# Optimization experiments

Measured on AMD Instinct MI355X. Metric: run time of the kernel, lower is better.

## Reference

```python
import jax, jax.numpy as jnp
import numpy as np

B, S, DIM, H, DH, DEPTH, NCLS = 4, 2048, 128, 8, 128, 2, 10
M = 128          # number of FAVOR+ random features
CHUNK = 128      # chunk size for causal linear attention
INNER = H * DH   # performer-pytorch: dim_head=dim -> inner_dim = heads*dim
FF = 4 * DIM


def layernorm(x, g, b, eps=1e-5):
    mu = jnp.mean(x, axis=-1, keepdims=True)
    var = jnp.mean((x - mu) ** 2, axis=-1, keepdims=True)
    return (x - mu) * jax.lax.rsqrt(var + eps) * g + b


def softmax_kernel(data, proj, is_query, eps=1e-4):
    # FAVOR+ positive softmax-kernel features. data: [B,H,S,DH], proj: [M,DH]
    norm = DH ** -0.25
    ratio = M ** -0.5
    d = data * norm
    dd = jnp.einsum('bhsd,md->bhsm', d, proj)
    diag = 0.5 * jnp.sum(d * d, axis=-1, keepdims=True)
    if is_query:
        stab = jnp.max(dd, axis=-1, keepdims=True)
    else:
        stab = jnp.max(dd, axis=(-2, -1), keepdims=True)
    stab = jax.lax.stop_gradient(stab)
    return ratio * (jnp.exp(dd - diag - stab) + eps)


def causal_linear_attention(qp, kp, v):
    # qp,kp: [B,H,S,M], v: [B,H,S,DH]; chunked prefix-sum causal linear attention
    b, h, s, m = qp.shape
    d = v.shape[-1]
    nc = s // CHUNK
    def to_chunks(t):
        return t.reshape(b, h, nc, CHUNK, -1).transpose(2, 0, 1, 3, 4)
    qc, kc, vc = to_chunks(qp), to_chunks(kp), to_chunks(v)
    tri = jnp.tril(jnp.ones((CHUNK, CHUNK), qp.dtype))
    def step(carry, inp):
        kv_sum, k_sum = carry           # [b,h,m,d], [b,h,m]
        qi, ki, vi = inp                # [b,h,CHUNK,*]
        attn = jnp.einsum('bhim,bhjm->bhij', qi, ki) * tri
        num = jnp.einsum('bhij,bhjd->bhid', attn, vi) \
            + jnp.einsum('bhim,bhmd->bhid', qi, kv_sum)
        den = jnp.sum(attn, axis=-1) + jnp.einsum('bhim,bhm->bhi', qi, k_sum)
        out = num / (den[..., None] + 1e-6)
        kv_sum = kv_sum + jnp.einsum('bhjm,bhjd->bhmd', ki, vi)
        k_sum = k_sum + jnp.sum(ki, axis=2)
        return (kv_sum, k_sum), out
    init = (jnp.zeros((b, h, m, d), qp.dtype), jnp.zeros((b, h, m), qp.dtype))
    _, out = jax.lax.scan(step, init, (qc, kc, vc))
    return out.transpose(1, 2, 0, 3, 4).reshape(b, h, s, d)


def setup_inputs():
    key = jax.random.key(0)
    ks = jax.random.split(key, 12)
    rng = np.random.default_rng(0)
    # sinusoidal positional encoding [S, DIM]
    pe = np.zeros((S, DIM), np.float32)
    pos = np.arange(S)[:, None].astype(np.float32)
    div = np.exp(np.arange(0, DIM, 2).astype(np.float32) * (-np.log(10000.0) / DIM))
    pe[:, 0::2] = np.sin(pos * div)
    pe[:, 1::2] = np.cos(pos * div)
    # orthogonal random feature projections per layer [DEPTH, M, DH]
    proj = np.stack([
        (np.linalg.qr(rng.standard_normal((DH, DH)))[0][:M] * np.sqrt(DH))
        for _ in range(DEPTH)
    ]).astype(np.float32)
    def gn(k, shape, scale):
        return jax.random.normal(k, shape, jnp.float32) * scale
    return {
        'x': gn(ks[0], (B, S, 1), 1.0),
        'lin_w': gn(ks[1], (1, DIM), 1.0),
        'lin_b': jnp.zeros((DIM,), jnp.float32),
        'pe': jnp.asarray(pe),
        'proj': jnp.asarray(proj),
        'ln1_g': jnp.ones((DEPTH, DIM), jnp.float32),
        'ln1_b': jnp.zeros((DEPTH, DIM), jnp.float32),
        'wq': gn(ks[2], (DEPTH, DIM, INNER), DIM ** -0.5),
        'wk': gn(ks[3], (DEPTH, DIM, INNER), DIM ** -0.5),
        'wv': gn(ks[4], (DEPTH, DIM, INNER), DIM ** -0.5),
        'wo': gn(ks[5], (DEPTH, INNER, DIM), INNER ** -0.5),
        'wo_b': jnp.zeros((DEPTH, DIM), jnp.float32),
        'ln2_g': jnp.ones((DEPTH, DIM), jnp.float32),
        'ln2_b': jnp.zeros((DEPTH, DIM), jnp.float32),
        'ff1_w': gn(ks[6], (DEPTH, DIM, FF), DIM ** -0.5),
        'ff1_b': jnp.zeros((DEPTH, FF), jnp.float32),
        'ff2_w': gn(ks[7], (DEPTH, FF, DIM), FF ** -0.5),
        'ff2_b': jnp.zeros((DEPTH, DIM), jnp.float32),
        'fin_w': gn(ks[8], (DIM, NCLS), DIM ** -0.5),
        'fin_b': jnp.zeros((NCLS,), jnp.float32),
    }


def reference(x, lin_w, lin_b, pe, proj, ln1_g, ln1_b, wq, wk, wv, wo, wo_b,
              ln2_g, ln2_b, ff1_w, ff1_b, ff2_w, ff2_b, fin_w, fin_b):
    h = x @ lin_w + lin_b            # [B,S,DIM]
    h = h + pe[None]
    for l in range(DEPTH):
        # --- pre-norm FAVOR+ causal self-attention ---
        y = layernorm(h, ln1_g[l], ln1_b[l])
        def split(t):  # [B,S,INNER] -> [B,H,S,DH]
            return t.reshape(B, S, H, DH).transpose(0, 2, 1, 3)
        q, k, v = split(y @ wq[l]), split(y @ wk[l]), split(y @ wv[l])
        qp = softmax_kernel(q, proj[l], True)
        kp = softmax_kernel(k, proj[l], False)
        o = causal_linear_attention(qp, kp, v)          # [B,H,S,DH]
        o = o.transpose(0, 2, 1, 3).reshape(B, S, INNER)
        h = h + (o @ wo[l] + wo_b[l])
        # --- pre-norm FFN ---
        y = layernorm(h, ln2_g[l], ln2_b[l])
        f = jax.nn.gelu(y @ ff1_w[l] + ff1_b[l]) @ ff2_w[l] + ff2_b[l]
        h = h + f
    pooled = jnp.mean(h, axis=1)     # [B,DIM]
    return pooled @ fin_w + fin_b    # [B,NCLS]
```

## Files before the change

### kernel.cpp

```cpp
#include <hip/hip_runtime.h>
#include <hip/hip_bf16.h>

#define Bb 4
#define Ss 2048
#define DIMc 128
#define Hh 8
#define DHc 128
#define Mf 128
#define CH 128
#define NCc 16
#define INNERc 1024
#define FFc 512

union F4 { float4 v; float f[4]; };
typedef unsigned short u16;

typedef __bf16 bf16x8 __attribute__((ext_vector_type(8)));
typedef float  f32x4  __attribute__((ext_vector_type(4)));

__device__ __forceinline__ unsigned fkey(float f){
  unsigned b = __float_as_uint(f);
  return (b & 0x80000000u) ? ~b : (b | 0x80000000u);
}
__device__ __forceinline__ float funkey(unsigned u){
  unsigned b = (u & 0x80000000u) ? (u & 0x7fffffffu) : ~u;
  return __uint_as_float(b);
}
__device__ __forceinline__ float gelu_f(float x){
  return 0.5f*x*(1.0f + tanhf(0.7978845608028654f*(x + 0.044715f*x*x*x)));
}
__device__ __forceinline__ u16 f2bu(float f){
  unsigned u = __float_as_uint(f);
  return (u16)((u + 0x7fffu + ((u>>16)&1u)) >> 16);
}
__device__ __forceinline__ float b2f(u16 u){
  return __uint_as_float(((unsigned)u)<<16);
}

__device__ __forceinline__ bf16x8 ldfrag(const u16* base, int row, int e){
  int byte = (row*256 + e*2) ^ ((row&7)<<4);
  return *(const bf16x8*)((const char*)base + byte);
}
__device__ __forceinline__ void stage_lin_bf(u16* dst, const u16* src, int srs, int t){
  #pragma unroll
  for(int it=0; it<8; ++it){
    int idx = t + it*256; int r = idx>>4, c8 = idx&15;
    int byte = (r*256 + c8*16) ^ ((r&7)<<4);
    *(uint4*)((char*)dst + byte) = *(const uint4*)(src + r*srs + c8*8);
  }
}
__device__ __forceinline__ void stage_lin_f32(u16* dst, const float* src, int srs, int t){
  #pragma unroll
  for(int it=0; it<8; ++it){
    int idx = t + it*256; int r = idx>>4, c8 = idx&15;
    F4 v0, v1;
    v0.v = *(const float4*)(src + r*srs + c8*8);
    v1.v = *(const float4*)(src + r*srs + c8*8 + 4);
    u16 tmp[8];
    #pragma unroll
    for(int u=0;u<4;u++){ tmp[u] = f2bu(v0.f[u]); tmp[4+u] = f2bu(v1.f[u]); }
    int byte = (r*256 + c8*16) ^ ((r&7)<<4);
    *(uint4*)((char*)dst + byte) = *(uint4*)tmp;
  }
}
__device__ __forceinline__ void stage_tr_bf(u16* dst, const u16* src, int srs, int t){
  int j0 = (t & 63)*2; int wv = t>>6;
  #pragma unroll
  for(int it=0; it<2; ++it){
    int d0 = wv*16 + it*64;
    u16 a0[16], a1[16];
    *(uint4*)&a0[0] = *(const uint4*)(src + j0*srs + d0);
    *(uint4*)&a0[8] = *(const uint4*)(src + j0*srs + d0 + 8);
    *(uint4*)&a1[0] = *(const uint4*)(src + (j0+1)*srs + d0);
    *(uint4*)&a1[8] = *(const uint4*)(src + (j0+1)*srs + d0 + 8);
    #pragma unroll
    for(int dc=0; dc<16; ++dc){
      int d = d0 + dc;
      unsigned pk = (unsigned)a0[dc] | ((unsigned)a1[dc]<<16);
      int byte = (d*256 + j0*2) ^ ((d&7)<<4);
      *(unsigned*)((char*)dst + byte) = pk;
    }
  }
}
__device__ __forceinline__ void stage_tr_f32(u16* dst, const float* src, int srs, int t){
  int j0 = (t & 63)*2; int wv = t>>6;
  #pragma unroll
  for(int it=0; it<2; ++it){
    int d0 = wv*16 + it*64;
    F4 r0[4], r1[4];
    #pragma unroll
    for(int u=0;u<4;u++){
      r0[u].v = *(const float4*)(src + j0*srs     + d0 + u*4);
      r1[u].v = *(const float4*)(src + (j0+1)*srs + d0 + u*4);
    }
    #pragma unroll
    for(int dc=0; dc<16; ++dc){
      int d = d0 + dc;
      unsigned pk = (unsigned)f2bu(r0[dc>>2].f[dc&3]) |
                    ((unsigned)f2bu(r1[dc>>2].f[dc&3])<<16);
      int byte = (d*256 + j0*2) ^ ((d&7)<<4);
      *(unsigned*)((char*)dst + byte) = pk;
    }
  }
}

__device__ __forceinline__ int2 swz_tile(){
  int nx = gridDim.x;
  int nwg = gridDim.x*gridDim.y;
  int lin = blockIdx.y*nx + blockIdx.x;
  int q = nwg>>3, r = nwg&7;
  int xcd = lin&7, idx = lin>>3;
  int nl = (xcd<r) ? (xcd*(q+1)+idx) : (r*(q+1)+(xcd-r)*q+idx);
  return make_int2(nl % nx, nl / nx);
}

__global__ __launch_bounds__(64) void k_init(unsigned* kstab){
  if(threadIdx.x < 64) kstab[threadIdx.x] = 0u;
}

__global__ __launch_bounds__(256) void k_embed(const float* __restrict__ x,
    const float* __restrict__ lw, const float* __restrict__ lb,
    const float* __restrict__ pe, float* __restrict__ h){
  int idx = blockIdx.x*256 + threadIdx.x;
  int d = idx & 127; int bs = idx >> 7; int s = bs & (Ss-1);
  h[idx] = x[bs]*lw[d] + lb[d] + pe[s*DIMc + d];
}

__global__ __launch_bounds__(256) void k_ln(const float* __restrict__ in,
    const float* __restrict__ g, const float* __restrict__ bta,
    u16* __restrict__ out){
  int wave = threadIdx.x >> 6; int lane = threadIdx.x & 63;
  int row = blockIdx.x*4 + wave;
  const float* r = in + row*DIMc;
  float x1 = r[lane], x2 = r[lane+64];
  float s = x1+x2, sq = x1*x1 + x2*x2;
  #pragma unroll
  for(int m=1;m<64;m<<=1){ s += __shfl_xor(s,m,64); sq += __shfl_xor(sq,m,64); }
  float mu = s * (1.0f/128.0f);
  float var = sq*(1.0f/128.0f) - mu*mu;
  float rs = rsqrtf(var + 1e-5f);
  out[row*DIMc+lane]    = f2bu((x1-mu)*rs*g[lane]+bta[lane]);
  out[row*DIMc+lane+64] = f2bu((x2-mu)*rs*g[lane+64]+bta[lane+64]);
}

template<bool BIAS, bool GELU, bool RES, bool OBF>
__global__ __launch_bounds__(256) void k_gemm_bf(const u16* __restrict__ A,
    const float* __restrict__ Bw, const float* __restrict__ bias,
    const float* __restrict__ resid, void* __restrict__ Cp, int N, int K){
  __shared__ u16 As[64][40];
  __shared__ u16 Bs[64][40];
  int2 tt = swz_tile();
  int n0 = tt.x*64, m0 = tt.y*64;
  int t = threadIdx.x; int wid = t>>6, lane = t&63;
  int wr = wid>>1, wc = wid&1;
  int fr = lane&15, kc = lane>>4;
  f32x4 acc[2][2] = {};
  for(int k0=0; k0<K; k0+=32){
    {
      int r = t>>2, c8 = t&3;
      *(uint4*)&As[r][c8*8] = *(const uint4*)(A + (m0+r)*K + k0 + c8*8);
    }
    {
      int n = t&63, c8 = t>>6;
      u16 tmp[8];
      #pragma unroll
      for(int j=0;j<8;j++) tmp[j] = f2bu(Bw[(k0 + c8*8 + j)*N + n0 + n]);
      *(uint4*)&Bs[n][c8*8] = *(uint4*)tmp;
    }
    __syncthreads();
    bf16x8 af[2], bf[2];
    #pragma unroll
    for(int i=0;i<2;i++) af[i] = *(const bf16x8*)&As[wr*32 + i*16 + fr][kc*8];
    #pragma unroll
    for(int j=0;j<2;j++) bf[j] = *(const bf16x8*)&Bs[wc*32 + j*16 + fr][kc*8];
    #pragma unroll
    for(int i=0;i<2;i++)
      #pragma unroll
      for(int j=0;j<2;j++)
        acc[i][j] = __builtin_amdgcn_mfma_f32_16x16x32_bf16(af[i], bf[j], acc[i][j], 0, 0, 0);
    __syncthreads();
  }
  #pragma unroll
  for(int i=0;i<2;i++){
    #pragma unroll
    for(int r=0;r<4;r++){
      int row = m0 + wr*32 + i*16 + kc*4 + r;
      #pragma unroll
      for(int j=0;j<2;j++){
        int col = n0 + wc*32 + j*16 + fr;
        float val = acc[i][j][r];
        if(BIAS) val += bias[col];
        if(GELU) val = gelu_f(val);
        if(RES)  val += resid[row*N+col];
        if(OBF) ((u16*)Cp)[row*N+col] = f2bu(val);
        else    ((float*)Cp)[row*N+col] = val;
      }
    }
  }
}

template<bool ISQ>
__global__ __launch_bounds__(256) void k_featm(
    const u16* xin, u16* qout, float* ktmp,
    const float* __restrict__ proj, unsigned* kstab){
  __shared__ __align__(16) u16 xs[16384];
  __shared__ __align__(16) u16 ps[16384];
  __shared__ float diag_s[128];
  __shared__ unsigned hmax[8];
  int r0 = blockIdx.x*128;
  int t = threadIdx.x; int lane = t&63, w = t>>6;
  int fr = lane&15, kc = lane>>4;
  const float norm  = 0.29730177875068026f;
  const float ratio = 0.08838834764831845f;
  if(!ISQ && t<8) hmax[t] = 0u;
  stage_lin_bf(xs, xin + (size_t)r0*128, 128, t);
  stage_lin_f32(ps, proj, 128, t);
  {
    int r = t>>1, half = t&1;
    const u16* rp = xin + (size_t)(r0+r)*128 + half*64;
    float ss = 0.f;
    #pragma unroll
    for(int u4=0; u4<8; ++u4){
      u16 tmp[8]; *(uint4*)tmp = *(const uint4*)(rp + u4*8);
      #pragma unroll
      for(int u=0;u<8;u++){ float f = b2f(tmp[u]); ss += f*f; }
    }
    ss += __shfl_xor(ss, 1, 64);
    if(half==0) diag_s[r] = 0.5f*norm*norm*ss;
  }
  __syncthreads();
  f32x4 acc[2][8] = {};
  #pragma unroll
  for(int ks=0; ks<4; ++ks){
    bf16x8 a[2];
    #pragma unroll
    for(int i=0;i<2;i++) a[i] = ldfrag(xs, w*32+i*16+fr, ks*32+kc*8);
    bf16x8 bm[8];
    #pragma unroll
    for(int cb=0;cb<8;cb++) bm[cb] = ldfrag(ps, cb*16+fr, ks*32+kc*8);
    #pragma unroll
    for(int i=0;i<2;i++)
      #pragma unroll
      for(int cb=0;cb<8;cb++)
        acc[i][cb] = __builtin_amdgcn_mfma_f32_16x16x32_bf16(a[i], bm[cb], acc[i][cb], 0,0,0);
  }
  __syncthreads();
  #pragma unroll
  for(int i=0;i<2;i++){
    #pragma unroll
    for(int r=0;r<4;r++){
      int row = w*32 + i*16 + kc*4 + r;
      float rmax = acc[i][0][r];
      #pragma unroll
      for(int cb=1;cb<8;cb++) rmax = fmaxf(rmax, acc[i][cb][r]);
      #pragma unroll
      for(int msk=1;msk<16;msk<<=1) rmax = fmaxf(rmax, __shfl_xor(rmax, msk, 64));
      float dg = diag_s[row];
      if(ISQ){
        float base = -dg - norm*rmax;
        #pragma unroll
        for(int cb=0;cb<8;cb++){
          float val = ratio*(expf(fmaf(norm, acc[i][cb][r], base)) + 1e-4f);
          int byte = (row*256 + (cb*16+fr)*2) ^ ((row&7)<<4);
          *(u16*)((char*)xs + byte) = f2bu(val);
        }
      } else {
        if(fr==0) atomicMax(&hmax[row&7], fkey(norm*rmax));
        float* kb = ktmp + (size_t)(r0+row)*128;
        #pragma unroll
        for(int cb=0;cb<8;cb++)
          kb[cb*16+fr] = fmaf(norm, acc[i][cb][r], -dg);
      }
    }
  }
  __syncthreads();
  if(ISQ){
    #pragma unroll
    for(int it=0; it<8; ++it){
      int idx = t + it*256; int r = idx>>4, c8 = idx&15;
      int byte = (r*256 + c8*16) ^ ((r&7)<<4);
      *(uint4*)(qout + (size_t)(r0+r)*128 + c8*8) = *(uint4*)((char*)xs + byte);
    }
  } else {
    int b = r0 >> 14;
    if(t<8) atomicMax(&kstab[b*8 + t], hmax[t]);
  }
}

__global__ __launch_bounds__(256) void k_kfeatB(const float* __restrict__ ktmp,
    u16* __restrict__ kp, const unsigned* __restrict__ kstab){
  const float ratio = 0.08838834764831845f;
  int idx8 = blockIdx.x*256 + threadIdx.x;
  int e = idx8*8;
  int row = e >> 7; int bh = ((row>>14)<<3) | (row & 7);
  float stab = funkey(kstab[bh]);
  F4 v0, v1;
  v0.v = *(const float4*)(ktmp+e);
  v1.v = *(const float4*)(ktmp+e+4);
  u16 ob[8];
  #pragma unroll
  for(int u=0;u<4;u++) ob[u]   = f2bu(ratio*(expf(v0.f[u] - stab)+1e-4f));
  #pragma unroll
  for(int u=0;u<4;u++) ob[4+u] = f2bu(ratio*(expf(v1.f[u] - stab)+1e-4f));
  *(uint4*)(kp+e) = *(uint4*)ob;
}

__global__ __launch_bounds__(256) void k_attn1m(const u16* __restrict__ kp,
    const u16* __restrict__ v, float* __restrict__ kvc, float* __restrict__ ksc){
  __shared__ __align__(16) u16 kt[16384];
  __shared__ __align__(16) u16 vt[16384];
  int bc = blockIdx.x; int c = bc&15, bh = bc>>4, b = bh>>3, hh = bh&7;
  int t = threadIdx.x; int lane = t&63, w = t>>6;
  int fr = lane&15, kc = lane>>4;
  int s0 = c*128;
  const u16* kb = kp + (size_t)((b*Ss+s0)*Hh + hh)*128;
  const u16* vb = v  + (size_t)((b*Ss+s0)*Hh + hh)*128;
  stage_tr_bf(kt, kb, 1024, t);
  stage_tr_bf(vt, vb, 1024, t);
  __syncthreads();
  f32x4 acc[2][8] = {};
  f32x4 ks[2] = {};
  bf16x8 bones;
  #pragma unroll
  for(int e=0;e<8;e++) bones[e] = (fr==0) ? (__bf16)1.0f : (__bf16)0.0f;
  #pragma unroll
  for(int js=0;js<4;js++){
    bf16x8 am[2];
    #pragma unroll
    for(int i=0;i<2;i++) am[i] = ldfrag(kt, w*32+i*16+fr, js*32+kc*8);
    bf16x8 bv[8];
    #pragma unroll
    for(int cb=0;cb<8;cb++) bv[cb] = ldfrag(vt, cb*16+fr, js*32+kc*8);
    #pragma unroll
    for(int i=0;i<2;i++){
      ks[i] = __builtin_amdgcn_mfma_f32_16x16x32_bf16(am[i], bones, ks[i], 0,0,0);
      #pragma unroll
      for(int cb=0;cb<8;cb++)
        acc[i][cb] = __builtin_amdgcn_mfma_f32_16x16x32_bf16(am[i], bv[cb], acc[i][cb], 0,0,0);
    }
  }
  float* kvb = kvc + (size_t)bc*16384;
  #pragma unroll
  for(int i=0;i<2;i++){
    #pragma unroll
    for(int r=0;r<4;r++){
      int m = w*32 + i*16 + kc*4 + r;
      #pragma unroll
      for(int cb=0;cb<8;cb++) kvb[m*128 + cb*16 + fr] = acc[i][cb][r];
      if(fr==0) ksc[bc*128 + m] = ks[i][r];
    }
  }
}

__global__ __launch_bounds__(256) void k_prefix(float* __restrict__ kvc){
  int bh = blockIdx.x >> 6; int pos = (blockIdx.x & 63)*256 + threadIdx.x;
  int base = bh*16*16384 + pos;
  float a = 0.f;
  #pragma unroll
  for(int c=0;c<16;c++){
    float xv = kvc[base + c*16384];
    kvc[base + c*16384] = a;
    a += xv;
  }
}
__global__ __launch_bounds__(256) void k_prefix_ks(float* __restrict__ ksc){
  int e = blockIdx.x*256 + threadIdx.x;
  int bh = e>>7, m = e&127;
  float a = 0.f;
  #pragma unroll
  for(int c=0;c<16;c++){
    int idx = (bh*16+c)*128 + m;
    float xv = ksc[idx]; ksc[idx] = a; a += xv;
  }
}

__global__ __launch_bounds__(256) void k_attn2m(const u16* __restrict__ qp,
    const u16* __restrict__ kp, const u16* __restrict__ v,
    const float* __restrict__ kvc, const float* __restrict__ ksc,
    u16* __restrict__ o){
  __shared__ __align__(16) u16 qs[16384];
  __shared__ __align__(16) u16 bs[16384];
  __shared__ float ksum_s[128];
  int bc = blockIdx.x; int c = bc&15, bh = bc>>4, b = bh>>3, hh = bh&7;
  int t = threadIdx.x; int lane = t&63, w = t>>6;
  int fr = lane&15, kc = lane>>4;
  int s0 = c*128;
  const u16* qb = qp + (size_t)((b*Ss+s0)*Hh + hh)*128;
  const u16* kb = kp + (size_t)((b*Ss+s0)*Hh + hh)*128;
  const u16* vb = v  + (size_t)((b*Ss+s0)*Hh + hh)*128;
  const float* kvb = kvc + (size_t)bc*16384;
  stage_lin_bf(qs, qb, 1024, t);
  stage_lin_bf(bs, kb, 1024, t);
  if(t<128) ksum_s[t] = ksc[bc*128 + t];
  __syncthreads();
  bf16x8 aq[2][4];
  #pragma unroll
  for(int i=0;i<2;i++)
    #pragma unroll
    for(int ks=0;ks<4;ks++)
      aq[i][ks] = ldfrag(qs, w*32+i*16+fr, ks*32+kc*8);
  f32x4 sacc[2][8] = {};
  #pragma unroll
  for(int ks=0;ks<4;ks++){
    bf16x8 bk[8];
    #pragma unroll
    for(int cb=0;cb<8;cb++) bk[cb] = ldfrag(bs, cb*16+fr, ks*32+kc*8);
    #pragma unroll
    for(int i=0;i<2;i++)
      #pragma unroll
      for(int cb=0;cb<8;cb++)
        sacc[i][cb] = __builtin_amdgcn_mfma_f32_16x16x32_bf16(aq[i][ks], bk[cb], sacc[i][cb], 0,0,0);
  }
  __syncthreads();
  #pragma unroll
  for(int i=0;i<2;i++){
    #pragma unroll
    for(int cb=0;cb<8;cb++){
      #pragma unroll
      for(int r=0;r<4;r++){
        int prow = w*32 + i*16 + kc*4 + r;
        int pcol = cb*16 + fr;
        float pv = (pcol > prow) ? 0.f : sacc[i][cb][r];
        int byte = (prow*256 + pcol*2) ^ ((prow&7)<<4);
        *(u16*)((char*)qs + byte) = f2bu(pv);
      }
    }
  }
  stage_tr_bf(bs, vb, 1024, t);
  __syncthreads();
  f32x4 nacc[2][8] = {};
  f32x4 dacc[2] = {};
  bf16x8 bones;
  #pragma unroll
  for(int e=0;e<8;e++) bones[e] = (fr==0) ? (__bf16)1.0f : (__bf16)0.0f;
  #pragma unroll
  for(int js=0;js<4;js++){
    bf16x8 ap[2];
    #pragma unroll
    for(int i=0;i<2;i++) ap[i] = ldfrag(qs, w*32+i*16+fr, js*32+kc*8);
    bf16x8 bv[8];
    #pragma unroll
    for(int cb=0;cb<8;cb++) bv[cb] = ldfrag(bs, cb*16+fr, js*32+kc*8);
    #pragma unroll
    for(int i=0;i<2;i++){
      dacc[i] = __builtin_amdgcn_mfma_f32_16x16x32_bf16(ap[i], bones, dacc[i], 0,0,0);
      #pragma unroll
      for(int cb=0;cb<8;cb++)
        nacc[i][cb] = __builtin_amdgcn_mfma_f32_16x16x32_bf16(ap[i], bv[cb], nacc[i][cb], 0,0,0);
    }
  }
  __syncthreads();
  stage_tr_f32(bs, kvb, 128, t);
  __syncthreads();
  #pragma unroll
  for(int ms=0;ms<4;ms++){
    bf16x8 bkv[8];
    #pragma unroll
    for(int cb=0;cb<8;cb++) bkv[cb] = ldfrag(bs, cb*16+fr, ms*32+kc*8);
    bf16x8 bks;
    #pragma unroll
    for(int e=0;e<8;e++) bks[e] = (fr==0) ? (__bf16)ksum_s[ms*32+kc*8+e] : (__bf16)0.0f;
    #pragma unroll
    for(int i=0;i<2;i++){
      dacc[i] = __builtin_amdgcn_mfma_f32_16x16x32_bf16(aq[i][ms], bks, dacc[i], 0,0,0);
      #pragma unroll
      for(int cb=0;cb<8;cb++)
        nacc[i][cb] = __builtin_amdgcn_mfma_f32_16x16x32_bf16(aq[i][ms], bkv[cb], nacc[i][cb], 0,0,0);
    }
  }
  #pragma unroll
  for(int i=0;i<2;i++){
    #pragma unroll
    for(int r=0;r<4;r++){
      float den = __shfl(dacc[i][r], lane & 48, 64);
      float inv = 1.0f/(den + 1e-6f);
      int row = w*32 + i*16 + kc*4 + r;
      u16* ob = o + (size_t)((b*Ss+s0+row)*Hh + hh)*128;
      #pragma unroll
      for(int cb=0;cb<8;cb++)
        ob[cb*16 + fr] = f2bu(nacc[i][cb][r] * inv);
    }
  }
}

__global__ __launch_bounds__(256) void k_pool(const float* __restrict__ h,
    float* __restrict__ pw){
  __shared__ float part[256];
  int blk = blockIdx.x; int b = blk>>4, c = blk&15;
  int t = threadIdx.x; int half = t>>7;
  float s = 0.f;
  int s0 = c*128 + half*64;
  for(int si=s0; si<s0+64; ++si) s += h[(b*Ss+si)*128 + (t&127)];
  part[t] = s;
  __syncthreads();
  if(t<128) pw[blk*128 + t] = part[t] + part[t+128];
}
__global__ __launch_bounds__(128) void k_cls(const float* __restrict__ pw,
    const float* __restrict__ fw, const float* __restrict__ fb,
    float* __restrict__ out){
  __shared__ float pool_s[128];
  int b = blockIdx.x; int t = threadIdx.x;
  float s = 0.f;
  for(int c=0;c<16;c++) s += pw[(b*16+c)*128 + t];
  pool_s[t] = s * (1.0f/2048.0f);
  __syncthreads();
  if(t<10){
    float a = fb[t];
    for(int d=0; d<128; ++d) a += pool_s[d]*fw[d*10+t];
    out[b*10+t] = a;
  }
}

extern "C" void kernel_launch(void* const* d_in, const int* in_sizes, int n_in,
                              void* d_out, int out_size, void* d_ws, size_t ws_size,
                              hipStream_t stream){
  (void)in_sizes; (void)n_in; (void)out_size; (void)ws_size;
  const float* x     = (const float*)d_in[0];
  const float* lin_w = (const float*)d_in[1];
  const float* lin_b = (const float*)d_in[2];
  const float* pe    = (const float*)d_in[3];
  const float* proj  = (const float*)d_in[4];
  const float* ln1_g = (const float*)d_in[5];
  const float* ln1_b = (const float*)d_in[6];
  const float* wq    = (const float*)d_in[7];
  const float* wk    = (const float*)d_in[8];
  const float* wv    = (const float*)d_in[9];
  const float* wo    = (const float*)d_in[10];
  const float* wo_b  = (const float*)d_in[11];
  const float* ln2_g = (const float*)d_in[12];
  const float* ln2_b = (const float*)d_in[13];
  const float* ff1w  = (const float*)d_in[14];
  const float* ff1b  = (const float*)d_in[15];
  const float* ff2w  = (const float*)d_in[16];
  const float* ff2b  = (const float*)d_in[17];
  const float* finw  = (const float*)d_in[18];
  const float* finb  = (const float*)d_in[19];
  float* out = (float*)d_out;

  float* ws  = (float*)d_ws;
  float* h    = ws;
  u16*  y    = (u16*)(h + 1048576);
  u16*  q    = (u16*)(h + 1048576 + 524288);
  u16*  k    = q + 8388608;
  u16*  v    = k + 8388608;
  u16*  o    = v + 8388608;
  float* ktmp = (float*)(o + 8388608);
  float* kvc  = ktmp + 8388608;
  float* ksc  = kvc + 8388608;
  float* pw   = ksc + 65536;
  unsigned* kstab = (unsigned*)(pw + 8192);

  k_init<<<1,64,0,stream>>>(kstab);
  k_embed<<<4096,256,0,stream>>>(x, lin_w, lin_b, pe, h);
  for(int l=0;l<2;l++){
    const float* projl = proj + l*Mf*DHc;
    k_ln<<<2048,256,0,stream>>>(h, ln1_g + l*DIMc, ln1_b + l*DIMc, y);
    k_gemm_bf<false,false,false,true><<<dim3(16,128),256,0,stream>>>(y, wq + l*DIMc*INNERc, nullptr, nullptr, q, INNERc, DIMc);
    k_gemm_bf<false,false,false,true><<<dim3(16,128),256,0,stream>>>(y, wk + l*DIMc*INNERc, nullptr, nullptr, k, INNERc, DIMc);
    k_gemm_bf<false,false,false,true><<<dim3(16,128),256,0,stream>>>(y, wv + l*DIMc*INNERc, nullptr, nullptr, v, INNERc, DIMc);
    k_featm<true><<<512,256,0,stream>>>(q, q, nullptr, projl, nullptr);
    k_featm<false><<<512,256,0,stream>>>(k, nullptr, ktmp, projl, kstab + l*32);
    k_kfeatB<<<4096,256,0,stream>>>(ktmp, k, kstab + l*32);
    k_attn1m<<<512,256,0,stream>>>(k, v, kvc, ksc);
    k_prefix<<<2048,256,0,stream>>>(kvc);
    k_prefix_ks<<<16,256,0,stream>>>(ksc);
    k_attn2m<<<512,256,0,stream>>>(q, k, v, kvc, ksc, o);
    k_gemm_bf<true,false,true,false><<<dim3(2,128),256,0,stream>>>(o, wo + l*INNERc*DIMc, wo_b + l*DIMc, h, h, DIMc, INNERc);
    k_ln<<<2048,256,0,stream>>>(h, ln2_g + l*DIMc, ln2_b + l*DIMc, y);
    k_gemm_bf<true,true,false,true><<<dim3(8,128),256,0,stream>>>(y, ff1w + l*DIMc*FFc, ff1b + l*FFc, nullptr, q, FFc, DIMc);
    k_gemm_bf<true,false,true,false><<<dim3(2,128),256,0,stream>>>(q, ff2w + l*FFc*DIMc, ff2b + l*DIMc, h, h, DIMc, FFc);
  }
  k_pool<<<64,256,0,stream>>>(h, pw);
  k_cls<<<4,128,0,stream>>>(pw, finw, finb, out);
}
```

Baseline: 487.7 us.

## Defer key-feature stabilization into attention kernels and store KV chunk state in bf16

The key feature kernel now writes exp(dd - diag) directly as bf16 instead of an fp32 temporary. The global max stabilizer and the ratio/eps terms are applied later as a scale and offset when keys are staged in the attention kernels, which removes the separate k_kfeatB pass and its fp32 round trip. The per-chunk KV sums and their prefix scan are also moved from fp32 to bf16, halving that traffic and the number of prefix blocks. The costs are a possible fp32 exp overflow without pre-subtracting the max, and lower precision in the accumulated prefix state.

```diff
diff --git a/kernel.cpp b/kernel.cpp
--- a/kernel.cpp
+++ b/kernel.cpp
@@ -49,6 +49,18 @@
     *(uint4*)((char*)dst + byte) = *(const uint4*)(src + r*srs + c8*8);
   }
 }
+__device__ __forceinline__ void stage_lin_bf_s(u16* dst, const u16* src, int srs,
+    int t, float sc, float off){
+  #pragma unroll
+  for(int it=0; it<8; ++it){
+    int idx = t + it*256; int r = idx>>4, c8 = idx&15;
+    u16 tmp[8]; *(uint4*)tmp = *(const uint4*)(src + r*srs + c8*8);
+    #pragma unroll
+    for(int u=0;u<8;u++) tmp[u] = f2bu(fmaf(b2f(tmp[u]), sc, off));
+    int byte = (r*256 + c8*16) ^ ((r&7)<<4);
+    *(uint4*)((char*)dst + byte) = *(uint4*)tmp;
+  }
+}
 __device__ __forceinline__ void stage_lin_f32(u16* dst, const float* src, int srs, int t){
   #pragma unroll
   for(int it=0; it<8; ++it){
@@ -82,22 +94,22 @@
     }
   }
 }
-__device__ __forceinline__ void stage_tr_f32(u16* dst, const float* src, int srs, int t){
+__device__ __forceinline__ void stage_tr_bf_s(u16* dst, const u16* src, int srs,
+    int t, float sc, float off){
   int j0 = (t & 63)*2; int wv = t>>6;
   #pragma unroll
   for(int it=0; it<2; ++it){
     int d0 = wv*16 + it*64;
-    F4 r0[4], r1[4];
-    #pragma unroll
-    for(int u=0;u<4;u++){
-      r0[u].v = *(const float4*)(src + j0*srs     + d0 + u*4);
-      r1[u].v = *(const float4*)(src + (j0+1)*srs + d0 + u*4);
-    }
+    u16 a0[16], a1[16];
+    *(uint4*)&a0[0] = *(const uint4*)(src + j0*srs + d0);
+    *(uint4*)&a0[8] = *(const uint4*)(src + j0*srs + d0 + 8);
+    *(uint4*)&a1[0] = *(const uint4*)(src + (j0+1)*srs + d0);
+    *(uint4*)&a1[8] = *(const uint4*)(src + (j0+1)*srs + d0 + 8);
     #pragma unroll
     for(int dc=0; dc<16; ++dc){
       int d = d0 + dc;
-      unsigned pk = (unsigned)f2bu(r0[dc>>2].f[dc&3]) |
-                    ((unsigned)f2bu(r1[dc>>2].f[dc&3])<<16);
+      unsigned pk = (unsigned)f2bu(fmaf(b2f(a0[dc]), sc, off)) |
+                    ((unsigned)f2bu(fmaf(b2f(a1[dc]), sc, off))<<16);
       int byte = (d*256 + j0*2) ^ ((d&7)<<4);
       *(unsigned*)((char*)dst + byte) = pk;
     }
@@ -201,8 +213,7 @@
 
 template<bool ISQ>
 __global__ __launch_bounds__(256) void k_featm(
-    const u16* xin, u16* qout, float* ktmp,
-    const float* __restrict__ proj, unsigned* kstab){
+    const u16* xin, u16* qout, const float* __restrict__ proj, unsigned* kstab){
   __shared__ __align__(16) u16 xs[16384];
   __shared__ __align__(16) u16 ps[16384];
   __shared__ float diag_s[128];
@@ -250,12 +261,12 @@
     #pragma unroll
     for(int r=0;r<4;r++){
       int row = w*32 + i*16 + kc*4 + r;
+      float dg = diag_s[row];
       float rmax = acc[i][0][r];
       #pragma unroll
       for(int cb=1;cb<8;cb++) rmax = fmaxf(rmax, acc[i][cb][r]);
       #pragma unroll
       for(int msk=1;msk<16;msk<<=1) rmax = fmaxf(rmax, __shfl_xor(rmax, msk, 64));
-      float dg = diag_s[row];
       if(ISQ){
         float base = -dg - norm*rmax;
         #pragma unroll
@@ -266,56 +277,44 @@
         }
       } else {
         if(fr==0) atomicMax(&hmax[row&7], fkey(norm*rmax));
-        float* kb = ktmp + (size_t)(r0+row)*128;
         #pragma unroll
-        for(int cb=0;cb<8;cb++)
-          kb[cb*16+fr] = fmaf(norm, acc[i][cb][r], -dg);
+        for(int cb=0;cb<8;cb++){
+          float val = expf(fmaf(norm, acc[i][cb][r], -dg));
+          int byte = (row*256 + (cb*16+fr)*2) ^ ((row&7)<<4);
+          *(u16*)((char*)xs + byte) = f2bu(val);
+        }
       }
     }
   }
   __syncthreads();
-  if(ISQ){
-    #pragma unroll
-    for(int it=0; it<8; ++it){
-      int idx = t + it*256; int r = idx>>4, c8 = idx&15;
-      int byte = (r*256 + c8*16) ^ ((r&7)<<4);
-      *(uint4*)(qout + (size_t)(r0+r)*128 + c8*8) = *(uint4*)((char*)xs + byte);
-    }
-  } else {
+  #pragma unroll
+  for(int it=0; it<8; ++it){
+    int idx = t + it*256; int r = idx>>4, c8 = idx&15;
+    int byte = (r*256 + c8*16) ^ ((r&7)<<4);
+    *(uint4*)(qout + (size_t)(r0+r)*128 + c8*8) = *(uint4*)((char*)xs + byte);
+  }
+  if(!ISQ){
     int b = r0 >> 14;
     if(t<8) atomicMax(&kstab[b*8 + t], hmax[t]);
   }
 }
 
-__global__ __launch_bounds__(256) void k_kfeatB(const float* __restrict__ ktmp,
-    u16* __restrict__ kp, const unsigned* __restrict__ kstab){
-  const float ratio = 0.08838834764831845f;
-  int idx8 = blockIdx.x*256 + threadIdx.x;
-  int e = idx8*8;
-  int row = e >> 7; int bh = ((row>>14)<<3) | (row & 7);
-  float stab = funkey(kstab[bh]);
-  F4 v0, v1;
-  v0.v = *(const float4*)(ktmp+e);
-  v1.v = *(const float4*)(ktmp+e+4);
-  u16 ob[8];
-  #pragma unroll
-  for(int u=0;u<4;u++) ob[u]   = f2bu(ratio*(expf(v0.f[u] - stab)+1e-4f));
-  #pragma unroll
-  for(int u=0;u<4;u++) ob[4+u] = f2bu(ratio*(expf(v1.f[u] - stab)+1e-4f));
-  *(uint4*)(kp+e) = *(uint4*)ob;
-}
-
 __global__ __launch_bounds__(256) void k_attn1m(const u16* __restrict__ kp,
-    const u16* __restrict__ v, float* __restrict__ kvc, float* __restrict__ ksc){
+    const u16* __restrict__ v, u16* __restrict__ kvc, float* __restrict__ ksc,
+    const unsigned* __restrict__ kstab){
   __shared__ __align__(16) u16 kt[16384];
   __shared__ __align__(16) u16 vt[16384];
   int bc = blockIdx.x; int c = bc&15, bh = bc>>4, b = bh>>3, hh = bh&7;
   int t = threadIdx.x; int lane = t&63, w = t>>6;
   int fr = lane&15, kc = lane>>4;
   int s0 = c*128;
+  const float ratio = 0.08838834764831845f;
+  float stab = funkey(kstab[bh]);
+  float csc = ratio * expf(-stab);
+  float reps = ratio * 1e-4f;
   const u16* kb = kp + (size_t)((b*Ss+s0)*Hh + hh)*128;
   const u16* vb = v  + (size_t)((b*Ss+s0)*Hh + hh)*128;
-  stage_tr_bf(kt, kb, 1024, t);
+  stage_tr_bf_s(kt, kb, 1024, t, csc, reps);
   stage_tr_bf(vt, vb, 1024, t);
   __syncthreads();
   f32x4 acc[2][8] = {};
@@ -339,28 +338,29 @@
         acc[i][cb] = __builtin_amdgcn_mfma_f32_16x16x32_bf16(am[i], bv[cb], acc[i][cb], 0,0,0);
     }
   }
-  float* kvb = kvc + (size_t)bc*16384;
+  u16* kvb = kvc + (size_t)bc*16384;
   #pragma unroll
   for(int i=0;i<2;i++){
     #pragma unroll
     for(int r=0;r<4;r++){
       int m = w*32 + i*16 + kc*4 + r;
       #pragma unroll
-      for(int cb=0;cb<8;cb++) kvb[m*128 + cb*16 + fr] = acc[i][cb][r];
+      for(int cb=0;cb<8;cb++) kvb[m*128 + cb*16 + fr] = f2bu(acc[i][cb][r]);
       if(fr==0) ksc[bc*128 + m] = ks[i][r];
     }
   }
 }
 
-__global__ __launch_bounds__(256) void k_prefix(float* __restrict__ kvc){
-  int bh = blockIdx.x >> 6; int pos = (blockIdx.x & 63)*256 + threadIdx.x;
-  int base = bh*16*16384 + pos;
-  float a = 0.f;
+__global__ __launch_bounds__(256) void k_prefix(unsigned* __restrict__ kvc){
+  int bh = blockIdx.x >> 5; int pos = (blockIdx.x & 31)*256 + threadIdx.x;
+  int base = bh*16*8192 + pos;
+  float a0 = 0.f, a1 = 0.f;
   #pragma unroll
   for(int c=0;c<16;c++){
-    float xv = kvc[base + c*16384];
-    kvc[base + c*16384] = a;
-    a += xv;
+    unsigned pk = kvc[base + c*8192];
+    float x0 = b2f((u16)pk), x1 = b2f((u16)(pk>>16));
+    kvc[base + c*8192] = (unsigned)f2bu(a0) | ((unsigned)f2bu(a1)<<16);
+    a0 += x0; a1 += x1;
   }
 }
 __global__ __launch_bounds__(256) void k_prefix_ks(float* __restrict__ ksc){
@@ -376,8 +376,8 @@
 
 __global__ __launch_bounds__(256) void k_attn2m(const u16* __restrict__ qp,
     const u16* __restrict__ kp, const u16* __restrict__ v,
-    const float* __restrict__ kvc, const float* __restrict__ ksc,
-    u16* __restrict__ o){
+    const u16* __restrict__ kvc, const float* __restrict__ ksc,
+    u16* __restrict__ o, const unsigned* __restrict__ kstab){
   __shared__ __align__(16) u16 qs[16384];
   __shared__ __align__(16) u16 bs[16384];
   __shared__ float ksum_s[128];
@@ -385,12 +385,16 @@
   int t = threadIdx.x; int lane = t&63, w = t>>6;
   int fr = lane&15, kc = lane>>4;
   int s0 = c*128;
+  const float ratio = 0.08838834764831845f;
+  float stab = funkey(kstab[bh]);
+  float csc = ratio * expf(-stab);
+  float reps = ratio * 1e-4f;
   const u16* qb = qp + (size_t)((b*Ss+s0)*Hh + hh)*128;
   const u16* kb = kp + (size_t)((b*Ss+s0)*Hh + hh)*128;
   const u16* vb = v  + (size_t)((b*Ss+s0)*Hh + hh)*128;
-  const float* kvb = kvc + (size_t)bc*16384;
+  const u16* kvb = kvc + (size_t)bc*16384;
   stage_lin_bf(qs, qb, 1024, t);
-  stage_lin_bf(bs, kb, 1024, t);
+  stage_lin_bf_s(bs, kb, 1024, t, csc, reps);
   if(t<128) ksum_s[t] = ksc[bc*128 + t];
   __syncthreads();
   bf16x8 aq[2][4];
@@ -450,7 +454,7 @@
     }
   }
   __syncthreads();
-  stage_tr_f32(bs, kvb, 128, t);
+  stage_tr_bf(bs, kvb, 128, t);
   __syncthreads();
   #pragma unroll
   for(int ms=0;ms<4;ms++){
@@ -544,9 +548,8 @@
   u16*  k    = q + 8388608;
   u16*  v    = k + 8388608;
   u16*  o    = v + 8388608;
-  float* ktmp = (float*)(o + 8388608);
-  float* kvc  = ktmp + 8388608;
-  float* ksc  = kvc + 8388608;
+  u16*  kvc  = o + 8388608;
+  float* ksc  = (float*)(kvc + 8388608);
   float* pw   = ksc + 65536;
   unsigned* kstab = (unsigned*)(pw + 8192);
 
@@ -558,13 +561,12 @@
     k_gemm_bf<false,false,false,true><<<dim3(16,128),256,0,stream>>>(y, wq + l*DIMc*INNERc, nullptr, nullptr, q, INNERc, DIMc);
     k_gemm_bf<false,false,false,true><<<dim3(16,128),256,0,stream>>>(y, wk + l*DIMc*INNERc, nullptr, nullptr, k, INNERc, DIMc);
     k_gemm_bf<false,false,false,true><<<dim3(16,128),256,0,stream>>>(y, wv + l*DIMc*INNERc, nullptr, nullptr, v, INNERc, DIMc);
-    k_featm<true><<<512,256,0,stream>>>(q, q, nullptr, projl, nullptr);
-    k_featm<false><<<512,256,0,stream>>>(k, nullptr, ktmp, projl, kstab + l*32);
-    k_kfeatB<<<4096,256,0,stream>>>(ktmp, k, kstab + l*32);
-    k_attn1m<<<512,256,0,stream>>>(k, v, kvc, ksc);
-    k_prefix<<<2048,256,0,stream>>>(kvc);
+    k_featm<true><<<512,256,0,stream>>>(q, q, projl, nullptr);
+    k_featm<false><<<512,256,0,stream>>>(k, k, projl, kstab + l*32);
+    k_attn1m<<<512,256,0,stream>>>(k, v, kvc, ksc, kstab + l*32);
+    k_prefix<<<1024,256,0,stream>>>((unsigned*)kvc);
     k_prefix_ks<<<16,256,0,stream>>>(ksc);
-    k_attn2m<<<512,256,0,stream>>>(q, k, v, kvc, ksc, o);
+    k_attn2m<<<512,256,0,stream>>>(q, k, v, kvc, ksc, o, kstab + l*32);
     k_gemm_bf<true,false,true,false><<<dim3(2,128),256,0,stream>>>(o, wo + l*INNERc*DIMc, wo_b + l*DIMc, h, h, DIMc, INNERc);
     k_ln<<<2048,256,0,stream>>>(h, ln2_g + l*DIMc, ln2_b + l*DIMc, y);
     k_gemm_bf<true,true,false,true><<<dim3(8,128),256,0,stream>>>(y, ff1w + l*DIMc*FFc, ff1b + l*FFc, nullptr, q, FFc, DIMc);
```

Measured after the change: 455.9 us. 6.5% less time.
